# Optimization experiments

Hardware: AMD Instinct MI355X
Metric: run time of the kernel (lower is better)

## Reference

```python
import jax, jax.numpy as jnp
import numpy as np

N_USERS = 100000
N_ITEMS = 50000
N_NODES = N_USERS + N_ITEMS
EMB_DIM = 64
N_EDGES = 1200000
N_LAYERS = 3


def setup_inputs() -> dict:
    key = jax.random.key(0)
    k1, k2, k3, k4, k5 = jax.random.split(key, 5)
    edge_row = jax.random.randint(k1, (N_EDGES,), 0, N_NODES, dtype=jnp.int32)
    edge_col = jax.random.randint(k2, (N_EDGES,), 0, N_NODES, dtype=jnp.int32)
    edge_weight = jax.random.uniform(k3, (N_EDGES,), dtype=jnp.float32)
    # xavier_uniform for nn.Embedding: bound = sqrt(6/(fan_in+fan_out))
    bu = float(np.sqrt(6.0 / (N_USERS + EMB_DIM)))
    bi = float(np.sqrt(6.0 / (N_ITEMS + EMB_DIM)))
    user_emb = jax.random.uniform(k4, (N_USERS, EMB_DIM), jnp.float32, -bu, bu)
    item_emb = jax.random.uniform(k5, (N_ITEMS, EMB_DIM), jnp.float32, -bi, bi)
    return {
        "edge_row": edge_row,
        "edge_col": edge_col,
        "edge_weight": edge_weight,
        "user_emb": user_emb,
        "item_emb": item_emb,
    }


def _spmm(edge_row, edge_col, edge_weight, x):
    # y[i] = sum_{e: row[e]==i} w[e] * x[col[e]]  (COO sparse @ dense)
    gathered = x[edge_col] * edge_weight[:, None]  # [E, d]
    return jax.ops.segment_sum(gathered, edge_row, num_segments=N_NODES)


def reference(edge_row, edge_col, edge_weight, user_emb, item_emb):
    x = jnp.concatenate([user_emb, item_emb], axis=0)  # [N, d]
    acc = x  # running sum over layer outputs (layer 0 = initial embeddings)
    for _ in range(N_LAYERS):
        x = _spmm(edge_row, edge_col, edge_weight, x)
        acc = acc + x
    mean_emb = acc / (N_LAYERS + 1)
    return mean_emb[:N_USERS], mean_emb[N_USERS:]
```

## Files before the change

### kernel.cpp

```cpp
#include <hip/hip_runtime.h>
#include <hip/hip_bf16.h>


#define EMB 64
#define BUCKET_SHIFT 9
#define BROWS (1 << BUCKET_SHIFT)
#define NBUCK_PAD 320
#define S1_CHUNK 2048
#define BCAP 4608
#define S2_CAP 12
#define SPMM_BLOCKS 2048

typedef _Float16 h8 __attribute__((ext_vector_type(8)));
typedef _Float16 h2v __attribute__((ext_vector_type(2)));
typedef float f2v __attribute__((ext_vector_type(2)));
typedef float f4 __attribute__((ext_vector_type(4)));
typedef int i2v __attribute__((ext_vector_type(2)));

union H8U { h8 v; h2v p[4]; };

__global__ void s1_convert(const int* __restrict__ row, const int* __restrict__ col,
                           const float* __restrict__ w, int* __restrict__ cursor1,
                           int2* __restrict__ tmp,
                           const float* __restrict__ ue, const float* __restrict__ ie,
                           h8* __restrict__ X0h, int nu_elems, int total8,
                           int E, int s1Blocks) {
    int t = threadIdx.x;
    if ((int)blockIdx.x < s1Blocks) {
        __shared__ int lcount[NBUCK_PAD];
        __shared__ int lbase[NBUCK_PAD];
        int c0 = blockIdx.x * S1_CHUNK;
        if (t < NBUCK_PAD) lcount[t] = 0;
        __syncthreads();
        int pkc[S1_CHUNK / 512];
        int cc[S1_CHUNK / 512];
        int rr[S1_CHUNK / 512];
        float ww[S1_CHUNK / 512];
        #pragma unroll
        for (int i = 0; i < S1_CHUNK / 512; i++) {
            int e = c0 + i * 512 + t;
            pkc[i] = -1;
            if (e < E) {
                int r = row[e];
                int b = r >> BUCKET_SHIFT;
                int rank = atomicAdd(&lcount[b], 1);
                pkc[i] = (b << 12) | rank;
                cc[i] = col[e];
                rr[i] = r & (BROWS - 1);
                ww[i] = w[e];
            }
        }
        __syncthreads();
        if (t < NBUCK_PAD) {
            int c = lcount[t];
            if (c) lbase[t] = atomicAdd(&cursor1[t], c);
        }
        __syncthreads();
        #pragma unroll
        for (int i = 0; i < S1_CHUNK / 512; i++) {
            if (pkc[i] >= 0) {
                int b = pkc[i] >> 12;
                int pos = lbase[b] + (pkc[i] & 4095);
                if (pos < BCAP)
                    tmp[(size_t)b * BCAP + pos] =
                        make_int2((cc[i] << BUCKET_SHIFT) | rr[i], __float_as_int(ww[i]));
            }
        }
    } else {
        int g = (blockIdx.x - s1Blocks) * 512 + t;
        if (g >= total8) return;
        int base = g << 3;
        const f4* src = (const f4*)((base < nu_elems) ? (ue + base)
                                                      : (ie + (base - nu_elems)));
        f4 a = src[0], b = src[1];
        h8 o;
        o[0] = (_Float16)a.x; o[1] = (_Float16)a.y; o[2] = (_Float16)a.z; o[3] = (_Float16)a.w;
        o[4] = (_Float16)b.x; o[5] = (_Float16)b.y; o[6] = (_Float16)b.z; o[7] = (_Float16)b.w;
        X0h[g] = o;
    }
}

__global__ void scatter2(const int* __restrict__ cursor1, const int2* __restrict__ tmp,
                         int2* __restrict__ cw, int* __restrict__ rbeg,
                         int* __restrict__ rend, int nrows) {
    __shared__ int cnt[BROWS];
    __shared__ int wS[8];
    int t = threadIdx.x;
    int j = blockIdx.x;
    int rowbase = j << BUCKET_SHIFT;
    int rows_here = nrows - rowbase;
    if (rows_here > BROWS) rows_here = BROWS;
    int num = cursor1[j];
    if (num > BCAP) num = BCAP;
    int base = j * BCAP;
    int iters = (num + 511) >> 9;

    cnt[t] = 0;
    __syncthreads();

    int pkc[S2_CAP];
    int rk[S2_CAP];
    int wv[S2_CAP];
    bool cached = (iters <= S2_CAP);
    if (cached) {
        for (int i = 0; i < iters; i++) {
            int p = i * 512 + t;
            pkc[i] = -1;
            if (p < num) {
                int2 rec = tmp[base + p];
                pkc[i] = rec.x;
                wv[i] = rec.y;
                rk[i] = atomicAdd(&cnt[rec.x & (BROWS - 1)], 1);
            }
        }
    } else {
        for (int p = t; p < num; p += 512)
            atomicAdd(&cnt[tmp[base + p].x & (BROWS - 1)], 1);
    }
    __syncthreads();

    int v = cnt[t];
    int lane = t & 63;
    int wave = t >> 6;
    int s = v;
    #pragma unroll
    for (int off = 1; off < 64; off <<= 1) {
        int tt = __shfl_up(s, off, 64);
        if (lane >= off) s += tt;
    }
    if (lane == 63) wS[wave] = s;
    __syncthreads();
    int woff = 0;
    for (int w = 0; w < wave; w++) woff += wS[w];
    int excl = woff + s - v;
    if (t < rows_here) {
        rbeg[rowbase + t] = base + excl;
        rend[rowbase + t] = base + excl + v;
    }
    __syncthreads();
    cnt[t] = excl;
    __syncthreads();

    if (cached) {
        for (int i = 0; i < iters; i++) {
            if (pkc[i] >= 0) {
                int r = pkc[i] & (BROWS - 1);
                cw[base + cnt[r] + rk[i]] = make_int2(pkc[i] >> BUCKET_SHIFT, wv[i]);
            }
        }
    } else {
        for (int p = t; p < num; p += 512) {
            int2 rec = tmp[base + p];
            int r = rec.x & (BROWS - 1);
            int pos = atomicAdd(&cnt[r], 1);
            cw[base + pos] = make_int2(rec.x >> BUCKET_SHIFT, rec.y);
        }
    }
}

template <bool LAST>
__global__ __launch_bounds__(256) void spmm_kernel(
        const int* __restrict__ rbeg, const int* __restrict__ rend,
        const i2v* __restrict__ cw,
        const h8* __restrict__ Xin, h8* __restrict__ Xout,
        const h8* __restrict__ X0, const h8* __restrict__ X1,
        float* __restrict__ out, int nrows) {
    int lane = threadIdx.x & 63;
    int g = lane >> 3;
    int l8 = lane & 7;
    int wv = (blockIdx.x * blockDim.x + threadIdx.x) >> 6;
    int totWaves = (gridDim.x * blockDim.x) >> 6;

    for (int base8 = wv * 8; base8 < nrows; base8 += totWaves * 8) {
        int row = base8 + g;
        bool valid = row < nrows;
        int beg = valid ? rbeg[row] : 0;
        int end = valid ? rend[row] : 0;

        f2v acc2[4];
        #pragma unroll
        for (int k = 0; k < 4; k++) acc2[k] = (f2v){0.f, 0.f};

        int e = beg;
        for (; e + 1 < end; e += 2) {
            i2v c0 = cw[e];
            i2v c1 = cw[e + 1];
            H8U v0, v1;
            v0.v = Xin[(c0.x << 3) + l8];
            v1.v = Xin[(c1.x << 3) + l8];
            float w0 = __int_as_float(c0.y);
            float w1 = __int_as_float(c1.y);
            f2v w0p = (f2v){w0, w0};
            f2v w1p = (f2v){w1, w1};
            #pragma unroll
            for (int k = 0; k < 4; k++) {
                acc2[k] += w0p * __builtin_convertvector(v0.p[k], f2v);
                acc2[k] += w1p * __builtin_convertvector(v1.p[k], f2v);
            }
        }
        if (e < end) {
            i2v c0 = cw[e];
            H8U v0;
            v0.v = Xin[(c0.x << 3) + l8];
            float w0 = __int_as_float(c0.y);
            f2v w0p = (f2v){w0, w0};
            #pragma unroll
            for (int k = 0; k < 4; k++)
                acc2[k] += w0p * __builtin_convertvector(v0.p[k], f2v);
        }

        float* a = (float*)acc2;
        if (valid) {
            if (LAST) {
                h8 x0 = X0[(row << 3) + l8];
                h8 v1 = X1[(row << 3) + l8];
                h8 v2 = Xin[(row << 3) + l8];
                int base = (row << 6) + (l8 << 3);
                f4 o0, o1;
                o0.x = 0.25f * ((float)x0[0] + (float)v1[0] + (float)v2[0] + a[0]);
                o0.y = 0.25f * ((float)x0[1] + (float)v1[1] + (float)v2[1] + a[1]);
                o0.z = 0.25f * ((float)x0[2] + (float)v1[2] + (float)v2[2] + a[2]);
                o0.w = 0.25f * ((float)x0[3] + (float)v1[3] + (float)v2[3] + a[3]);
                o1.x = 0.25f * ((float)x0[4] + (float)v1[4] + (float)v2[4] + a[4]);
                o1.y = 0.25f * ((float)x0[5] + (float)v1[5] + (float)v2[5] + a[5]);
                o1.z = 0.25f * ((float)x0[6] + (float)v1[6] + (float)v2[6] + a[6]);
                o1.w = 0.25f * ((float)x0[7] + (float)v1[7] + (float)v2[7] + a[7]);
                f4* dst = (f4*)(out + base);
                dst[0] = o0;
                dst[1] = o1;
            } else {
                h8 o;
                #pragma unroll
                for (int k = 0; k < 8; k++) o[k] = (_Float16)a[k];
                Xout[(row << 3) + l8] = o;
            }
        }
    }
}

extern "C" void kernel_launch(void* const* d_in, const int* in_sizes, int n_in,
                              void* d_out, int out_size, void* d_ws, size_t ws_size,
                              hipStream_t stream) {
    const int* edge_row = (const int*)d_in[0];
    const int* edge_col = (const int*)d_in[1];
    const float* edge_w = (const float*)d_in[2];
    const float* user_emb = (const float*)d_in[3];
    const float* item_emb = (const float*)d_in[4];

    const int E = in_sizes[0];
    const int nu_elems = in_sizes[3];
    const int ni_elems = in_sizes[4];
    const int total = nu_elems + ni_elems;
    const int N = total / EMB;
    const int NBUCK = (N + BROWS - 1) >> BUCKET_SHIFT;

    size_t off = 0;
    auto carve = [&](size_t bytes) {
        void* p = (char*)d_ws + off;
        off += (bytes + 255) & ~(size_t)255;
        return p;
    };
    h8*    X0h     = (h8*)carve((size_t)total * 2);
    h8*    X1h     = (h8*)carve((size_t)total * 2);
    h8*    X2h     = (h8*)carve((size_t)total * 2);
    int*   rbeg    = (int*)carve((size_t)N * 4);
    int*   rend    = (int*)carve((size_t)N * 4);
    int*   cursor1 = (int*)carve((size_t)NBUCK * 4);
    int2*  tmp     = (int2*)carve((size_t)NBUCK * BCAP * 8);
    int2*  cw      = (int2*)carve((size_t)NBUCK * BCAP * 8);
    (void)ws_size;

    float* out = (float*)d_out;

    const int total8 = total / 8;
    const int s1Blocks = (E + S1_CHUNK - 1) / S1_CHUNK;
    const int convBlocks = (total8 + 511) / 512;

    hipMemsetAsync(cursor1, 0, (size_t)NBUCK * 4, stream);
    s1_convert<<<s1Blocks + convBlocks, 512, 0, stream>>>(
        edge_row, edge_col, edge_w, cursor1, tmp,
        user_emb, item_emb, X0h, nu_elems, total8, E, s1Blocks);
    scatter2<<<NBUCK, 512, 0, stream>>>(cursor1, tmp, cw, rbeg, rend, N);

    spmm_kernel<false><<<SPMM_BLOCKS, 256, 0, stream>>>(rbeg, rend, (const i2v*)cw,
                                                        X0h, X1h, nullptr, nullptr,
                                                        nullptr, N);
    spmm_kernel<false><<<SPMM_BLOCKS, 256, 0, stream>>>(rbeg, rend, (const i2v*)cw,
                                                        X1h, X2h, nullptr, nullptr,
                                                        nullptr, N);
    spmm_kernel<true><<<SPMM_BLOCKS, 256, 0, stream>>>(rbeg, rend, (const i2v*)cw,
                                                       X2h, nullptr, X0h, X1h,
                                                       out, N);
}
```

Before: 229.7 us.

## Replace two-pass bucket sort with global row histogram, scan, and atomic placement

The CSR build changes from bucketing edges into a temporary buffer and then re-sorting each bucket in shared memory. It now builds a per-row global histogram with atomics, scans it per bucket to get row offsets, and places each edge directly into its final slot with a global atomic cursor. This drops the temporary buffer round-trip and the shared-memory re-sort, at the cost of about 2.4M global atomics on row counters. Edge order within a row becomes nondeterministic, which can change fp summation order.

```diff
diff --git a/kernel.cpp b/kernel.cpp
--- a/kernel.cpp
+++ b/kernel.cpp
@@ -5,10 +5,7 @@
 #define EMB 64
 #define BUCKET_SHIFT 9
 #define BROWS (1 << BUCKET_SHIFT)
-#define NBUCK_PAD 320
-#define S1_CHUNK 2048
 #define BCAP 4608
-#define S2_CAP 12
 #define SPMM_BLOCKS 2048
 
 typedef _Float16 h8 __attribute__((ext_vector_type(8)));
@@ -19,55 +16,24 @@
 
 union H8U { h8 v; h2v p[4]; };
 
-__global__ void s1_convert(const int* __restrict__ row, const int* __restrict__ col,
-                           const float* __restrict__ w, int* __restrict__ cursor1,
-                           int2* __restrict__ tmp,
-                           const float* __restrict__ ue, const float* __restrict__ ie,
-                           h8* __restrict__ X0h, int nu_elems, int total8,
-                           int E, int s1Blocks) {
+__global__ void hist_convert(const int* __restrict__ row, int* __restrict__ rowcnt,
+                             const float* __restrict__ ue, const float* __restrict__ ie,
+                             h8* __restrict__ X0h, int nu_elems, int total8,
+                             int E, int histBlocks) {
     int t = threadIdx.x;
-    if ((int)blockIdx.x < s1Blocks) {
-        __shared__ int lcount[NBUCK_PAD];
-        __shared__ int lbase[NBUCK_PAD];
-        int c0 = blockIdx.x * S1_CHUNK;
-        if (t < NBUCK_PAD) lcount[t] = 0;
-        __syncthreads();
-        int pkc[S1_CHUNK / 512];
-        int cc[S1_CHUNK / 512];
-        int rr[S1_CHUNK / 512];
-        float ww[S1_CHUNK / 512];
-        #pragma unroll
-        for (int i = 0; i < S1_CHUNK / 512; i++) {
-            int e = c0 + i * 512 + t;
-            pkc[i] = -1;
-            if (e < E) {
-                int r = row[e];
-                int b = r >> BUCKET_SHIFT;
-                int rank = atomicAdd(&lcount[b], 1);
-                pkc[i] = (b << 12) | rank;
-                cc[i] = col[e];
-                rr[i] = r & (BROWS - 1);
-                ww[i] = w[e];
-            }
-        }
-        __syncthreads();
-        if (t < NBUCK_PAD) {
-            int c = lcount[t];
-            if (c) lbase[t] = atomicAdd(&cursor1[t], c);
-        }
-        __syncthreads();
-        #pragma unroll
-        for (int i = 0; i < S1_CHUNK / 512; i++) {
-            if (pkc[i] >= 0) {
-                int b = pkc[i] >> 12;
-                int pos = lbase[b] + (pkc[i] & 4095);
-                if (pos < BCAP)
-                    tmp[(size_t)b * BCAP + pos] =
-                        make_int2((cc[i] << BUCKET_SHIFT) | rr[i], __float_as_int(ww[i]));
-            }
+    if ((int)blockIdx.x < histBlocks) {
+        int idx4 = (blockIdx.x * 512 + t) * 4;
+        if (idx4 + 3 < E) {
+            int4 r4 = *(const int4*)(row + idx4);
+            atomicAdd(&rowcnt[r4.x], 1);
+            atomicAdd(&rowcnt[r4.y], 1);
+            atomicAdd(&rowcnt[r4.z], 1);
+            atomicAdd(&rowcnt[r4.w], 1);
+        } else {
+            for (int e = idx4; e < E; e++) atomicAdd(&rowcnt[row[e]], 1);
         }
     } else {
-        int g = (blockIdx.x - s1Blocks) * 512 + t;
+        int g = (blockIdx.x - histBlocks) * 512 + t;
         if (g >= total8) return;
         int base = g << 3;
         const f4* src = (const f4*)((base < nu_elems) ? (ue + base)
@@ -80,46 +46,14 @@
     }
 }
 
-__global__ void scatter2(const int* __restrict__ cursor1, const int2* __restrict__ tmp,
-                         int2* __restrict__ cw, int* __restrict__ rbeg,
-                         int* __restrict__ rend, int nrows) {
-    __shared__ int cnt[BROWS];
+__global__ void scan_rbeg(int* __restrict__ rowcnt, int* __restrict__ rbeg,
+                          int* __restrict__ rend, int nrows) {
     __shared__ int wS[8];
     int t = threadIdx.x;
     int j = blockIdx.x;
-    int rowbase = j << BUCKET_SHIFT;
-    int rows_here = nrows - rowbase;
-    if (rows_here > BROWS) rows_here = BROWS;
-    int num = cursor1[j];
-    if (num > BCAP) num = BCAP;
+    int row = (j << BUCKET_SHIFT) + t;
     int base = j * BCAP;
-    int iters = (num + 511) >> 9;
-
-    cnt[t] = 0;
-    __syncthreads();
-
-    int pkc[S2_CAP];
-    int rk[S2_CAP];
-    int wv[S2_CAP];
-    bool cached = (iters <= S2_CAP);
-    if (cached) {
-        for (int i = 0; i < iters; i++) {
-            int p = i * 512 + t;
-            pkc[i] = -1;
-            if (p < num) {
-                int2 rec = tmp[base + p];
-                pkc[i] = rec.x;
-                wv[i] = rec.y;
-                rk[i] = atomicAdd(&cnt[rec.x & (BROWS - 1)], 1);
-            }
-        }
-    } else {
-        for (int p = t; p < num; p += 512)
-            atomicAdd(&cnt[tmp[base + p].x & (BROWS - 1)], 1);
-    }
-    __syncthreads();
-
-    int v = cnt[t];
+    int v = (row < nrows) ? rowcnt[row] : 0;
     int lane = t & 63;
     int wave = t >> 6;
     int s = v;
@@ -133,27 +67,40 @@
     int woff = 0;
     for (int w = 0; w < wave; w++) woff += wS[w];
     int excl = woff + s - v;
-    if (t < rows_here) {
-        rbeg[rowbase + t] = base + excl;
-        rend[rowbase + t] = base + excl + v;
-    }
-    __syncthreads();
-    cnt[t] = excl;
-    __syncthreads();
-
-    if (cached) {
-        for (int i = 0; i < iters; i++) {
-            if (pkc[i] >= 0) {
-                int r = pkc[i] & (BROWS - 1);
-                cw[base + cnt[r] + rk[i]] = make_int2(pkc[i] >> BUCKET_SHIFT, wv[i]);
-            }
-        }
+    if (row < nrows) {
+        int rb = base + excl;
+        int re = rb + v;
+        int cap = base + BCAP;
+        if (rb > cap) rb = cap;
+        if (re > cap) re = cap;
+        rbeg[row] = rb;
+        rend[row] = re;
+        rowcnt[row] = rb;
+    }
+}
+
+__global__ void place_kernel(const int* __restrict__ row, const int* __restrict__ col,
+                             const float* __restrict__ w, int* __restrict__ cursor,
+                             int2* __restrict__ cw, int E) {
+    int idx4 = (blockIdx.x * blockDim.x + threadIdx.x) * 4;
+    if (idx4 + 3 < E) {
+        int4 r4 = *(const int4*)(row + idx4);
+        int4 c4 = *(const int4*)(col + idx4);
+        f4 w4 = *(const f4*)(w + idx4);
+        int p0 = atomicAdd(&cursor[r4.x], 1);
+        int p1 = atomicAdd(&cursor[r4.y], 1);
+        int p2 = atomicAdd(&cursor[r4.z], 1);
+        int p3 = atomicAdd(&cursor[r4.w], 1);
+        if (p0 < ((r4.x >> BUCKET_SHIFT) + 1) * BCAP) cw[p0] = make_int2(c4.x, __float_as_int(w4.x));
+        if (p1 < ((r4.y >> BUCKET_SHIFT) + 1) * BCAP) cw[p1] = make_int2(c4.y, __float_as_int(w4.y));
+        if (p2 < ((r4.z >> BUCKET_SHIFT) + 1) * BCAP) cw[p2] = make_int2(c4.z, __float_as_int(w4.z));
+        if (p3 < ((r4.w >> BUCKET_SHIFT) + 1) * BCAP) cw[p3] = make_int2(c4.w, __float_as_int(w4.w));
     } else {
-        for (int p = t; p < num; p += 512) {
-            int2 rec = tmp[base + p];
-            int r = rec.x & (BROWS - 1);
-            int pos = atomicAdd(&cnt[r], 1);
-            cw[base + pos] = make_int2(rec.x >> BUCKET_SHIFT, rec.y);
+        for (int e = idx4; e < E; e++) {
+            int r = row[e];
+            int pos = atomicAdd(&cursor[r], 1);
+            if (pos < ((r >> BUCKET_SHIFT) + 1) * BCAP)
+                cw[pos] = make_int2(col[e], __float_as_int(w[e]));
         }
     }
 }
@@ -265,22 +212,23 @@
     h8*    X2h     = (h8*)carve((size_t)total * 2);
     int*   rbeg    = (int*)carve((size_t)N * 4);
     int*   rend    = (int*)carve((size_t)N * 4);
-    int*   cursor1 = (int*)carve((size_t)NBUCK * 4);
-    int2*  tmp     = (int2*)carve((size_t)NBUCK * BCAP * 8);
+    int*   rowcnt  = (int*)carve((size_t)N * 4);
     int2*  cw      = (int2*)carve((size_t)NBUCK * BCAP * 8);
     (void)ws_size;
 
     float* out = (float*)d_out;
 
     const int total8 = total / 8;
-    const int s1Blocks = (E + S1_CHUNK - 1) / S1_CHUNK;
+    const int histBlocks = (E + 2047) / 2048;
     const int convBlocks = (total8 + 511) / 512;
-
-    hipMemsetAsync(cursor1, 0, (size_t)NBUCK * 4, stream);
-    s1_convert<<<s1Blocks + convBlocks, 512, 0, stream>>>(
-        edge_row, edge_col, edge_w, cursor1, tmp,
-        user_emb, item_emb, X0h, nu_elems, total8, E, s1Blocks);
-    scatter2<<<NBUCK, 512, 0, stream>>>(cursor1, tmp, cw, rbeg, rend, N);
+    const int placeBlocks = (E + 2047) / 2048;
+
+    hipMemsetAsync(rowcnt, 0, (size_t)N * 4, stream);
+    hist_convert<<<histBlocks + convBlocks, 512, 0, stream>>>(
+        edge_row, rowcnt, user_emb, item_emb, X0h, nu_elems, total8, E, histBlocks);
+    scan_rbeg<<<NBUCK, 512, 0, stream>>>(rowcnt, rbeg, rend, N);
+    place_kernel<<<placeBlocks, 512, 0, stream>>>(edge_row, edge_col, edge_w,
+                                                  rowcnt, cw, E);
 
     spmm_kernel<false><<<SPMM_BLOCKS, 256, 0, stream>>>(rbeg, rend, (const i2v*)cw,
                                                         X0h, X1h, nullptr, nullptr,
```

After: 331.1 us. 44.1% more time.
